# Performance work log

Hardware: AMD Instinct MI355X
Metric: run time of the kernel (lower is better)

## Reference

```python
import jax, jax.numpy as jnp
import numpy as np

N_NODES = 100_000
N_EDGES = 1_600_000
N_GRAPHS = 512
HID = 64
NUM_CLASSES = 100
VOCAB = 3100
ID_OFFSET = 1500
BN_EPS = 1e-5


def setup_inputs() -> dict:
    key = jax.random.key(0)
    ks = jax.random.split(key, 8)
    node_ids = jax.random.randint(ks[0], (N_NODES,), 0, 1600)
    edge_src = jax.random.randint(ks[1], (N_EDGES,), 0, N_NODES)
    edge_dst = jax.random.randint(ks[2], (N_EDGES,), 0, N_NODES)
    graph_ids = jnp.sort(jax.random.randint(ks[3], (N_NODES,), 0, N_GRAPHS))
    emb = jax.random.normal(ks[4], (VOCAB, HID), dtype=jnp.float32) * 0.02
    # 3 GIN layers x 3 MLP linear layers, all 64->64 since embedding_dim == hidden
    Ws = jax.random.normal(ks[5], (3, 3, HID, HID), dtype=jnp.float32) * 0.05
    bs = jnp.zeros((3, 3, HID), dtype=jnp.float32)
    bn_gamma = jnp.ones((3, HID), dtype=jnp.float32)
    bn_beta = jnp.zeros((3, HID), dtype=jnp.float32)
    eps = jnp.zeros((3,), dtype=jnp.float32)  # learn_eps=True, init 0
    W_out = jax.random.normal(ks[6], (3 * HID, NUM_CLASSES), dtype=jnp.float32) * 0.05
    b_out = jnp.zeros((NUM_CLASSES,), dtype=jnp.float32)
    return {"node_ids": node_ids, "edge_src": edge_src, "edge_dst": edge_dst,
            "graph_ids": graph_ids, "emb": emb, "Ws": Ws, "bs": bs,
            "bn_gamma": bn_gamma, "bn_beta": bn_beta, "eps": eps,
            "W_out": W_out, "b_out": b_out}


def reference(node_ids, edge_src, edge_dst, graph_ids, emb, Ws, bs,
              bn_gamma, bn_beta, eps, W_out, b_out):
    n = node_ids.shape[0]
    h = emb[node_ids + ID_OFFSET]  # [N, HID]
    pooled = []
    for l in range(3):  # GIN layers (fixed small count)
        # GINConv, sum aggregator: (1+eps)*h + sum over in-edges of h[src]
        agg = jax.ops.segment_sum(h[edge_src], edge_dst, num_segments=n)
        x = (1.0 + eps[l]) * h + agg
        for m in range(3):
            x = jax.nn.relu(x @ Ws[l, m] + bs[l, m])
        mean = x.mean(axis=0)
        var = x.var(axis=0)  # biased var, as torch BN uses for normalization
        x = (x - mean) * jax.lax.rsqrt(var + BN_EPS) * bn_gamma[l] + bn_beta[l]
        h = x
        # dgl.sum_nodes: per-graph segment sum
        pooled.append(jax.ops.segment_sum(h, graph_ids, num_segments=N_GRAPHS))
    graph_features = jnp.concatenate(pooled, axis=-1)  # [G, 3*HID]
    return graph_features @ W_out + b_out  # [G, NUM_CLASSES]
```

## Files before the change

### kernel.cpp

```cpp
#include <hip/hip_runtime.h>

#define N_NODES 100000
#define N_EDGES 1600000
#define N_GRAPHS 512
#define HID 64
#define NUM_CLASSES 100
#define ID_OFFSET 1500
#define BN_EPS 1e-5f
#define CAP 64
#define NBKT 256
#define BSHIFT 9
#define NUSED ((N_NODES + 511) >> 9)
#define BCAP 10240
#define CBLK 98
#define CHUNK 16384
#define WPBLK 5
#define EMBBLK ((N_NODES * 32 + 1023) / 1024)
#define DUMMY_ROW 100000

typedef __attribute__((ext_vector_type(8))) short short8;
typedef __attribute__((ext_vector_type(4))) float floatx4;

__device__ __forceinline__ float b2f(unsigned short u) {
    return __builtin_bit_cast(float, ((unsigned)u) << 16);
}
__device__ __forceinline__ unsigned short f2b(float f) {
    unsigned x = __builtin_bit_cast(unsigned, f);
    x += 0x7FFFu + ((x >> 16) & 1u);
    return (unsigned short)(x >> 16);
}

#define XSH(row, qq) ((((((row) >> 4) << 7) + ((qq) << 4) + (((row) & 15) ^ (qq))) * 8))


__global__ __launch_bounds__(1024) void prep_kernel(const int* __restrict__ src,
                                                    const int* __restrict__ dst,
                                                    int* __restrict__ cursor,
                                                    int* __restrict__ rec,
                                                    const float* __restrict__ Ws,
                                                    unsigned short* __restrict__ whi,
                                                    unsigned short* __restrict__ wlo,
                                                    const int* __restrict__ node_ids,
                                                    const int* __restrict__ gid,
                                                    const float* __restrict__ emb,
                                                    unsigned short* __restrict__ h,
                                                    unsigned short* __restrict__ xin,
                                                    int* __restrict__ gs,
                                                    int* __restrict__ ge) {
    __shared__ int hist[NBKT];
    __shared__ int base_s[NBKT];
    int t = threadIdx.x;
    int blk = blockIdx.x;

    if (blk < CBLK) {
        if (blk == 0 && t < 32) {
            ((unsigned*)(h + (size_t)DUMMY_ROW * 64))[t] = 0u;
            ((unsigned*)(xin + (size_t)DUMMY_ROW * 64))[t] = 0u;
        }
        if (t < NBKT) hist[t] = 0;
        __syncthreads();
        int cb = blk * CHUNK;
        int d_[16], s_[16];
#pragma unroll
        for (int k = 0; k < 16; ++k) {
            int i = cb + k * 1024 + t;
            d_[k] = (i < N_EDGES) ? dst[i] : -1;
            s_[k] = (i < N_EDGES) ? src[i] : 0;
            if (d_[k] >= 0) atomicAdd(&hist[((unsigned)d_[k] >> BSHIFT) & (NBKT - 1)], 1);
        }
        __syncthreads();
        if (t < NBKT) base_s[t] = (hist[t] > 0) ? atomicAdd(&cursor[t], hist[t]) : 0;
        __syncthreads();
        if (t < NBKT) hist[t] = 0;
        __syncthreads();
#pragma unroll
        for (int k = 0; k < 16; ++k) {
            if (d_[k] >= 0) {
                unsigned d = (unsigned)d_[k];
                int b = (d >> BSHIFT) & (NBKT - 1);
                int p = atomicAdd(&hist[b], 1);
                int g = base_s[b] + p;
                if ((unsigned)g < BCAP)
                    rec[b * BCAP + g] = ((int)(d & 511) << 17) | (s_[k] & 0x1FFFF);
            }
        }
    } else if (blk < CBLK + WPBLK) {
        int G = (blk - CBLK) * 1024 + t;
        if (G < 3 * 1536) {
            int l = G / 1536, Gp = G % 1536;
            int mm = Gp >> 9, rem = Gp & 511;
            int kq = rem >> 6, n = rem & 63;
            const float* Wp = Ws + l * 12288 + mm * 4096 + (kq * 8) * 64 + n;
            unsigned short uh[8], ul[8];
#pragma unroll
            for (int j = 0; j < 8; ++j) {
                float w = Wp[j * 64];
                unsigned short hi = f2b(w);
                uh[j] = hi;
                ul[j] = f2b(w - b2f(hi));
            }
            size_t off = (size_t)l * 12288 + (mm << 12) + XSH(n, kq);
            *(short8*)&whi[off] = *(short8*)uh;
            *(short8*)&wlo[off] = *(short8*)ul;
        }
    } else {
        int idx = (blk - CBLK - WPBLK) * 1024 + t;
        if (idx < N_NODES * 32) {
            int n = idx >> 5, cp = idx & 31;
            const float2 e = *(const float2*)(emb + (((size_t)(node_ids[n] + ID_OFFSET)) << 6) + cp * 2);
            unsigned v = (unsigned)f2b(e.x) | ((unsigned)f2b(e.y) << 16);
            ((unsigned*)h)[n * 32 + cp] = v;
            if (cp == 0) {
                int g = gid[n] & (N_GRAPHS - 1);
                if (n == 0 || (gid[n - 1] & (N_GRAPHS - 1)) != g) gs[g] = n;
                if (n == N_NODES - 1 || (gid[n + 1] & (N_GRAPHS - 1)) != g) ge[g] = n + 1;
            }
        }
    }
}


__global__ __launch_bounds__(1024) void fill_kernel(const int* __restrict__ rec,
                                                    const int* __restrict__ cursor,
                                                    int* __restrict__ cnt,
                                                    int* __restrict__ srcs) {
    __shared__ int lcnt[512];
    int t = threadIdx.x;
    int b = blockIdx.x;
    if (t < 512) lcnt[t] = 0;
    __syncthreads();
    int nb = cursor[b];
    if (nb < 0) nb = 0;
    if (nb > BCAP) nb = BCAP;
    const int* seg = rec + b * BCAP;
    for (int i = t; i < nb; i += 1024) {
        unsigned r = (unsigned)seg[i];
        int dl = (int)((r >> 17) & 511);
        int s = (int)(r & 0x1FFFF);
        int node = (b << BSHIFT) + dl;
        int p = atomicAdd(&lcnt[dl], 1);
        if (p < CAP && node < N_NODES) srcs[(node << 6) + p] = s;
    }
    __syncthreads();
    if (t < 512) {
        int node = (b << BSHIFT) + t;
        if (node < N_NODES) {
            int deg = lcnt[t];
            cnt[node] = deg;
            int degc = deg > CAP ? CAP : deg;
            int degp = (degc + 15) & ~15;
            if (degp < 32) degp = 32;
            for (int p = degc; p < degp; ++p) srcs[(node << 6) + p] = DUMMY_ROW;
        }
    }
}


__global__ __launch_bounds__(256, 4) void fused_kernel(const unsigned short* __restrict__ x,
                                                       unsigned short* __restrict__ xo,
                                                       const int* __restrict__ cnt,
                                                       const int* __restrict__ srcs,
                                                       const float* __restrict__ eps, int l,
                                                       float* __restrict__ stats,
                                                       const float* __restrict__ gamma,
                                                       const float* __restrict__ beta,
                                                       const unsigned short* __restrict__ whi,
                                                       const unsigned short* __restrict__ wlo,
                                                       const float* __restrict__ bs,
                                                       const int* __restrict__ graph_ids,
                                                       float* __restrict__ pooled, int last) {
    __shared__ __align__(16) unsigned short xs[64 * 64];
    __shared__ int garr[64];
    __shared__ float ssum[256], sqq[256];
    int t = threadIdx.x;
    int nodebase = blockIdx.x * 64;
    int lane = t & 63, w = t >> 6;
    int half = lane >> 5, cl = lane & 31;
    const unsigned* __restrict__ xu = (const unsigned*)x;

    if (lane < 16) {
        int n = nodebase + w * 16 + lane;
        garr[w * 16 + lane] = (n < N_NODES) ? (graph_ids[n] & (N_GRAPHS - 1)) : -1;
    }

    float scale = 1.0f + eps[l];
    float a0f = 1.0f, a1f = 1.0f, b0f = 0.0f, b1f = 0.0f;
    if (l > 0) {
        int lp = l - 1;
        float2 sm = *(const float2*)&stats[lp * 128 + 2 * cl];
        float2 sq = *(const float2*)&stats[lp * 128 + 64 + 2 * cl];
        float2 gm = *(const float2*)&gamma[lp * 64 + 2 * cl];
        float2 bt = *(const float2*)&beta[lp * 64 + 2 * cl];
        float mean0 = sm.x * (1.0f / N_NODES);
        float var0 = sq.x * (1.0f / N_NODES) - mean0 * mean0;
        float r0 = rsqrtf(var0 + BN_EPS);
        a0f = gm.x * r0;
        b0f = bt.x - mean0 * a0f;
        float mean1 = sm.y * (1.0f / N_NODES);
        float var1 = sq.y * (1.0f / N_NODES) - mean1 * mean1;
        float r1 = rsqrtf(var1 + BN_EPS);
        a1f = gm.y * r1;
        b1f = bt.y - mean1 * a1f;
    }

    int wb = __builtin_amdgcn_readfirstlane(nodebase + w * 16);

    for (int g4 = 0; g4 < 4; ++g4) {
        int nb = wb + g4 * 4;
        int deg[4], degp[4];
        const int* row[4];
#pragma unroll
        for (int n = 0; n < 4; ++n) {
            int d = (nb + n < N_NODES) ? cnt[nb + n] : 0;
            int dc = d < 0 ? 0 : (d > CAP ? CAP : d);
            deg[n] = dc;
            int dp = (dc + 15) & ~15;
            degp[n] = dp < 32 ? 32 : dp;
            row[n] = srcs + ((size_t)(nb + n) << 6);
        }
        int cmax = degp[0];
        cmax = degp[1] > cmax ? degp[1] : cmax;
        cmax = degp[2] > cmax ? degp[2] : cmax;
        cmax = degp[3] > cmax ? degp[3] : cmax;

        unsigned us[4];
#pragma unroll
        for (int n = 0; n < 4; ++n) us[n] = xu[(size_t)(nb + n) * 32 + cl];

        float A0[4] = {0.f, 0.f, 0.f, 0.f}, A1[4] = {0.f, 0.f, 0.f, 0.f};
        float B0[4] = {0.f, 0.f, 0.f, 0.f}, B1[4] = {0.f, 0.f, 0.f, 0.f};

        {
            unsigned uv[4][16];
#pragma unroll
            for (int n = 0; n < 4; ++n)
#pragma unroll
                for (int k = 0; k < 16; ++k) {
                    int ia = row[n][2 * k] & 0x1FFFF;
                    int ib = row[n][2 * k + 1] & 0x1FFFF;
                    int idx = half ? ib : ia;
                    uv[n][k] = xu[(size_t)idx * 32 + cl];
                }
#pragma unroll
            for (int n = 0; n < 4; ++n)
#pragma unroll
                for (int k = 0; k < 16; ++k) {
                    float lo = b2f((unsigned short)(uv[n][k] & 0xFFFF));
                    float hi = b2f((unsigned short)(uv[n][k] >> 16));
                    if (k & 1) { B0[n] += lo; B1[n] += hi; }
                    else       { A0[n] += lo; A1[n] += hi; }
                }
        }
        for (int c = 32; c < cmax; c += 16) {
            unsigned uc[4][8];
#pragma unroll
            for (int n = 0; n < 4; ++n)
                if (c < degp[n])
#pragma unroll
                    for (int k = 0; k < 8; ++k) {
                        int ia = row[n][c + 2 * k] & 0x1FFFF;
                        int ib = row[n][c + 2 * k + 1] & 0x1FFFF;
                        int idx = half ? ib : ia;
                        uc[n][k] = xu[(size_t)idx * 32 + cl];
                    }
#pragma unroll
            for (int n = 0; n < 4; ++n)
                if (c < degp[n])
#pragma unroll
                    for (int k = 0; k < 8; ++k) {
                        float lo = b2f((unsigned short)(uc[n][k] & 0xFFFF));
                        float hi = b2f((unsigned short)(uc[n][k] >> 16));
                        if (k & 1) { B0[n] += lo; B1[n] += hi; }
                        else       { A0[n] += lo; A1[n] += hi; }
                    }
        }

#pragma unroll
        for (int n = 0; n < 4; ++n) {
            float S0 = A0[n] + B0[n];
            float S1 = A1[n] + B1[n];
            S0 += __shfl_xor(S0, 32);
            S1 += __shfl_xor(S1, 32);
            if (half == 0) {
                float selflo = b2f((unsigned short)(us[n] & 0xFFFF));
                float selfhi = b2f((unsigned short)(us[n] >> 16));
                float db = scale + (float)deg[n];
                float v0 = fmaf(a0f, fmaf(scale, selflo, S0), db * b0f);
                float v1 = fmaf(a1f, fmaf(scale, selfhi, S1), db * b1f);
                int r = w * 16 + g4 * 4 + n;
                int col = 2 * cl;
                *(unsigned*)&xs[XSH(r, col >> 3) + (col & 7)] =
                    (unsigned)f2b(v0) | ((unsigned)f2b(v1) << 16);
            }
        }
    }

    int m = lane & 15, q = lane >> 4;
    const float* bb = bs + l * 3 * 64;
    const unsigned short* whil = whi + (size_t)l * 12288;
    const unsigned short* wlol = wlo + (size_t)l * 12288;
    for (int mm = 0; mm < 3; ++mm) {
        short8 bl[2][4];
#pragma unroll
        for (int kc = 0; kc < 2; ++kc)
#pragma unroll
            for (int tj = 0; tj < 4; ++tj)
                bl[kc][tj] = *(const short8*)&wlol[(mm << 12) + XSH(tj * 16 + m, kc * 4 + q)];
        short8 a[2];
#pragma unroll
        for (int kc = 0; kc < 2; ++kc)
            a[kc] = *(const short8*)&xs[XSH(w * 16 + m, kc * 4 + q)];

        floatx4 acc[4];
#pragma unroll
        for (int tj = 0; tj < 4; ++tj) {
            float bv = bb[mm * 64 + tj * 16 + m];
            acc[tj] = (floatx4){bv, bv, bv, bv};
        }
#pragma unroll
        for (int kc = 0; kc < 2; ++kc) {
            short8 bh[4];
#pragma unroll
            for (int tj = 0; tj < 4; ++tj)
                bh[tj] = *(const short8*)&whil[(mm << 12) + XSH(tj * 16 + m, kc * 4 + q)];
#pragma unroll
            for (int tj = 0; tj < 4; ++tj)
                acc[tj] = __builtin_amdgcn_mfma_f32_16x16x32_bf16(a[kc], bh[tj], acc[tj], 0, 0, 0);
        }
#pragma unroll
        for (int kc = 0; kc < 2; ++kc)
#pragma unroll
            for (int tj = 0; tj < 4; ++tj)
                acc[tj] = __builtin_amdgcn_mfma_f32_16x16x32_bf16(a[kc], bl[kc][tj], acc[tj], 0, 0, 0);
#pragma unroll
        for (int tj = 0; tj < 4; ++tj) {
            int col = tj * 16 + m;
#pragma unroll
            for (int r = 0; r < 4; ++r) {
                int row = w * 16 + q * 4 + r;
                float v = acc[tj][r];
                xs[XSH(row, col >> 3) + (col & 7)] = f2b(v > 0.f ? v : 0.f);
            }
        }
    }

    if (!last) {
        unsigned* xou = (unsigned*)xo;
#pragma unroll
        for (int it = 0; it < 8; ++it) {
            int row = w * 16 + (lane >> 5) + it * 2;
            int cp = lane & 31;
            int col = cp * 2;
            unsigned val = *(const unsigned*)&xs[XSH(row, col >> 3) + (col & 7)];
            int node = nodebase + row;
            if (node < N_NODES) xou[(size_t)node * 32 + cp] = val;
        }
    }
    {
        int c = lane;
        float s = 0.f, q2 = 0.f, acc2 = 0.f;
        int cur = -1;
        for (int k = 0; k < 16; ++k) {
            int row = w * 16 + k;
            int g = garr[row];
            if (g >= 0) {
                float v = b2f(xs[XSH(row, c >> 3) + (c & 7)]);
                s += v;
                q2 += v * v;
                if (g != cur) {
                    if (cur >= 0) atomicAdd(&pooled[cur * 192 + l * 64 + c], acc2);
                    acc2 = 0.f;
                    cur = g;
                }
                acc2 += v;
            }
        }
        if (cur >= 0) atomicAdd(&pooled[cur * 192 + l * 64 + c], acc2);
        ssum[t] = s;
        sqq[t] = q2;
    }
    __syncthreads();
    if (t < 64) {
        float S = ssum[t] + ssum[t + 64] + ssum[t + 128] + ssum[t + 192];
        float Q = sqq[t] + sqq[t + 64] + sqq[t + 128] + sqq[t + 192];
        atomicAdd(&stats[l * 128 + t], S);
        atomicAdd(&stats[l * 128 + 64 + t], Q);
    }
}


__global__ __launch_bounds__(256) void out_kernel(const float* __restrict__ pooled,
                                                  const float* __restrict__ stats,
                                                  const float* __restrict__ gamma,
                                                  const float* __restrict__ beta,
                                                  const int* __restrict__ gs,
                                                  const int* __restrict__ ge,
                                                  const float* __restrict__ Wo,
                                                  const float* __restrict__ bo,
                                                  float* __restrict__ out) {
    __shared__ float sab[384];
    int t = threadIdx.x;
    if (t < 192) {
        int l2 = t / 64, c = t & 63;
        float mean = stats[l2 * 128 + c] * (1.0f / N_NODES);
        float var = stats[l2 * 128 + 64 + c] * (1.0f / N_NODES) - mean * mean;
        float rstd = rsqrtf(var + BN_EPS);
        float a = gamma[l2 * 64 + c] * rstd;
        sab[l2 * 128 + c] = a;
        sab[l2 * 128 + 64 + c] = beta[l2 * 64 + c] - mean * a;
    }
    __syncthreads();
    int idx = blockIdx.x * blockDim.x + t;
    if (idx < N_GRAPHS * NUM_CLASSES) {
        int g = idx / NUM_CLASSES, k = idx % NUM_CLASSES;
        float cg = (float)(ge[g] - gs[g]);
        float acc = bo[k];
        for (int l2 = 0; l2 < 3; ++l2)
            for (int c = 0; c < 64; ++c) {
                float gf = fmaf(sab[l2 * 128 + c], pooled[g * 192 + l2 * 64 + c],
                                sab[l2 * 128 + 64 + c] * cg);
                acc = fmaf(gf, Wo[(l2 * 64 + c) * NUM_CLASSES + k], acc);
            }
        out[idx] = acc;
    }
}

extern "C" void kernel_launch(void* const* d_in, const int* in_sizes, int n_in,
                              void* d_out, int out_size, void* d_ws, size_t ws_size,
                              hipStream_t stream) {
    const int*   node_ids  = (const int*)d_in[0];
    const int*   edge_src  = (const int*)d_in[1];
    const int*   edge_dst  = (const int*)d_in[2];
    const int*   graph_ids = (const int*)d_in[3];
    const float* emb       = (const float*)d_in[4];
    const float* Ws        = (const float*)d_in[5];
    const float* bs        = (const float*)d_in[6];
    const float* gamma     = (const float*)d_in[7];
    const float* beta      = (const float*)d_in[8];
    const float* eps       = (const float*)d_in[9];
    const float* W_out     = (const float*)d_in[10];
    const float* b_out     = (const float*)d_in[11];
    float* out = (float*)d_out;

    unsigned short* h    = (unsigned short*)d_ws;
    unsigned short* xin  = h + 6400000 + 8192;
    unsigned short* whi  = xin + 6400000 + 8192;
    unsigned short* wlo  = whi + 36864;
    int*   srcs   = (int*)(wlo + 36864);
    int*   rec    = srcs + 6400000;
    float* pooled = (float*)(rec + NUSED * BCAP);
    float* stats  = pooled + 98304;
    int*   cnt    = (int*)(stats + 384);
    int*   gs     = cnt + 100000;
    int*   ge     = gs + 512;
    int*   cursor = ge + 512;

    hipMemsetAsync(pooled, 0,
                   (size_t)(98304 + 384 + 100000 + 512 + 512 + 256) * 4, stream);

    prep_kernel<<<CBLK + WPBLK + EMBBLK, 1024, 0, stream>>>(
        edge_src, edge_dst, cursor, rec, Ws, whi, wlo,
        node_ids, graph_ids, emb, h, xin, gs, ge);
    fill_kernel<<<NUSED, 1024, 0, stream>>>(rec, cursor, cnt, srcs);

    const int FUSE_BLK = (N_NODES + 63) / 64;
    for (int l = 0; l < 3; ++l) {
        const unsigned short* X = (l % 2 == 0) ? h : xin;
        unsigned short* A = (l % 2 == 0) ? xin : h;
        fused_kernel<<<FUSE_BLK, 256, 0, stream>>>(
            X, A, cnt, srcs, eps, l, stats, gamma, beta,
            whi, wlo, bs, graph_ids, pooled, l == 2);
    }

    out_kernel<<<(N_GRAPHS * NUM_CLASSES + 255) / 256, 256, 0, stream>>>(
        pooled, stats, gamma, beta, gs, ge, W_out, b_out, out);
}
```

Measured before the change: 349.4 us.

## Shrink fused GIN blocks to 16 nodes and replicate BN stat accumulators

Each fused block now handles 16 nodes instead of 64, so there are four times as many blocks, more parallelism and a smaller LDS footprint. The MLP is restructured so all four waves compute column tiles of a single 16-row tile, with double-buffered LDS and barriers between stages, and only one wave writes each result. BatchNorm sum and sum-of-squares atomics are spread over 16 replicated accumulators to reduce contention, and readers sum the replicas. The cost is redundant MFMA work across waves, extra __syncthreads, and four times as many stat atomics and prologue loads.

```diff
diff --git a/kernel.cpp b/kernel.cpp
--- a/kernel.cpp
+++ b/kernel.cpp
@@ -17,6 +17,8 @@
 #define WPBLK 5
 #define EMBBLK ((N_NODES * 32 + 1023) / 1024)
 #define DUMMY_ROW 100000
+#define SREP 16
+#define SSTRIDE 384
 
 typedef __attribute__((ext_vector_type(8))) short short8;
 typedef __attribute__((ext_vector_type(4))) float floatx4;
@@ -169,49 +171,52 @@
                                                        const float* __restrict__ bs,
                                                        const int* __restrict__ graph_ids,
                                                        float* __restrict__ pooled, int last) {
-    __shared__ __align__(16) unsigned short xs[64 * 64];
-    __shared__ int garr[64];
+    __shared__ __align__(16) unsigned short xs[2 * 16 * 64];
+    __shared__ int garr[16];
     __shared__ float ssum[256], sqq[256];
     int t = threadIdx.x;
-    int nodebase = blockIdx.x * 64;
+    int nodebase = blockIdx.x * 16;
     int lane = t & 63, w = t >> 6;
     int half = lane >> 5, cl = lane & 31;
     const unsigned* __restrict__ xu = (const unsigned*)x;
 
-    if (lane < 16) {
-        int n = nodebase + w * 16 + lane;
-        garr[w * 16 + lane] = (n < N_NODES) ? (graph_ids[n] & (N_GRAPHS - 1)) : -1;
-    }
+    if (t < 16) garr[t] = graph_ids[nodebase + t] & (N_GRAPHS - 1);
 
     float scale = 1.0f + eps[l];
     float a0f = 1.0f, a1f = 1.0f, b0f = 0.0f, b1f = 0.0f;
     if (l > 0) {
         int lp = l - 1;
-        float2 sm = *(const float2*)&stats[lp * 128 + 2 * cl];
-        float2 sq = *(const float2*)&stats[lp * 128 + 64 + 2 * cl];
+        float sm0 = 0.f, sm1 = 0.f, sq0 = 0.f, sq1 = 0.f;
+#pragma unroll
+        for (int rp = 0; rp < SREP; ++rp) {
+            const float* sp = stats + rp * SSTRIDE + lp * 128;
+            float2 a_ = *(const float2*)&sp[2 * cl];
+            float2 b_ = *(const float2*)&sp[64 + 2 * cl];
+            sm0 += a_.x; sm1 += a_.y;
+            sq0 += b_.x; sq1 += b_.y;
+        }
         float2 gm = *(const float2*)&gamma[lp * 64 + 2 * cl];
         float2 bt = *(const float2*)&beta[lp * 64 + 2 * cl];
-        float mean0 = sm.x * (1.0f / N_NODES);
-        float var0 = sq.x * (1.0f / N_NODES) - mean0 * mean0;
+        float mean0 = sm0 * (1.0f / N_NODES);
+        float var0 = sq0 * (1.0f / N_NODES) - mean0 * mean0;
         float r0 = rsqrtf(var0 + BN_EPS);
         a0f = gm.x * r0;
         b0f = bt.x - mean0 * a0f;
-        float mean1 = sm.y * (1.0f / N_NODES);
-        float var1 = sq.y * (1.0f / N_NODES) - mean1 * mean1;
+        float mean1 = sm1 * (1.0f / N_NODES);
+        float var1 = sq1 * (1.0f / N_NODES) - mean1 * mean1;
         float r1 = rsqrtf(var1 + BN_EPS);
         a1f = gm.y * r1;
         b1f = bt.y - mean1 * a1f;
     }
 
-    int wb = __builtin_amdgcn_readfirstlane(nodebase + w * 16);
-
-    for (int g4 = 0; g4 < 4; ++g4) {
-        int nb = wb + g4 * 4;
+    int nb = __builtin_amdgcn_readfirstlane(nodebase + w * 4);
+
+    {
         int deg[4], degp[4];
         const int* row[4];
 #pragma unroll
         for (int n = 0; n < 4; ++n) {
-            int d = (nb + n < N_NODES) ? cnt[nb + n] : 0;
+            int d = cnt[nb + n];
             int dc = d < 0 ? 0 : (d > CAP ? CAP : d);
             deg[n] = dc;
             int dp = (dc + 15) & ~15;
@@ -287,19 +292,22 @@
                 float db = scale + (float)deg[n];
                 float v0 = fmaf(a0f, fmaf(scale, selflo, S0), db * b0f);
                 float v1 = fmaf(a1f, fmaf(scale, selfhi, S1), db * b1f);
-                int r = w * 16 + g4 * 4 + n;
+                int r = w * 4 + n;
                 int col = 2 * cl;
                 *(unsigned*)&xs[XSH(r, col >> 3) + (col & 7)] =
                     (unsigned)f2b(v0) | ((unsigned)f2b(v1) << 16);
             }
         }
     }
+    __syncthreads();
 
     int m = lane & 15, q = lane >> 4;
     const float* bb = bs + l * 3 * 64;
     const unsigned short* whil = whi + (size_t)l * 12288;
     const unsigned short* wlol = wlo + (size_t)l * 12288;
     for (int mm = 0; mm < 3; ++mm) {
+        unsigned short* xr = xs + (mm & 1) * 1024;
+        unsigned short* xw = xs + ((mm & 1) ^ 1) * 1024;
         short8 bl[2][4];
 #pragma unroll
         for (int kc = 0; kc < 2; ++kc)
@@ -309,7 +317,7 @@
         short8 a[2];
 #pragma unroll
         for (int kc = 0; kc < 2; ++kc)
-            a[kc] = *(const short8*)&xs[XSH(w * 16 + m, kc * 4 + q)];
+            a[kc] = *(const short8*)&xr[XSH(m, kc * 4 + q)];
 
         floatx4 acc[4];
 #pragma unroll
@@ -335,45 +343,48 @@
 #pragma unroll
         for (int tj = 0; tj < 4; ++tj) {
             int col = tj * 16 + m;
-#pragma unroll
-            for (int r = 0; r < 4; ++r) {
-                int row = w * 16 + q * 4 + r;
-                float v = acc[tj][r];
-                xs[XSH(row, col >> 3) + (col & 7)] = f2b(v > 0.f ? v : 0.f);
-            }
-        }
-    }
+            if (q == w) {
+#pragma unroll
+                for (int r = 0; r < 4; ++r) {
+                    int row = q * 4 + r;
+                    float v = acc[tj][r];
+                    xw[XSH(row, col >> 3) + (col & 7)] = f2b(v > 0.f ? v : 0.f);
+                }
+            }
+        }
+        __syncthreads();
+    }
+
+    unsigned short* xf = xs + 1024;
 
     if (!last) {
         unsigned* xou = (unsigned*)xo;
 #pragma unroll
-        for (int it = 0; it < 8; ++it) {
-            int row = w * 16 + (lane >> 5) + it * 2;
+        for (int it = 0; it < 2; ++it) {
+            int row = w * 4 + (lane >> 5) + it * 2;
             int cp = lane & 31;
             int col = cp * 2;
-            unsigned val = *(const unsigned*)&xs[XSH(row, col >> 3) + (col & 7)];
-            int node = nodebase + row;
-            if (node < N_NODES) xou[(size_t)node * 32 + cp] = val;
+            unsigned val = *(const unsigned*)&xf[XSH(row, col >> 3) + (col & 7)];
+            xou[(size_t)(nodebase + row) * 32 + cp] = val;
         }
     }
     {
         int c = lane;
         float s = 0.f, q2 = 0.f, acc2 = 0.f;
         int cur = -1;
-        for (int k = 0; k < 16; ++k) {
-            int row = w * 16 + k;
+#pragma unroll
+        for (int k = 0; k < 4; ++k) {
+            int row = w * 4 + k;
             int g = garr[row];
-            if (g >= 0) {
-                float v = b2f(xs[XSH(row, c >> 3) + (c & 7)]);
-                s += v;
-                q2 += v * v;
-                if (g != cur) {
-                    if (cur >= 0) atomicAdd(&pooled[cur * 192 + l * 64 + c], acc2);
-                    acc2 = 0.f;
-                    cur = g;
-                }
-                acc2 += v;
-            }
+            float v = b2f(xf[XSH(row, c >> 3) + (c & 7)]);
+            s += v;
+            q2 += v * v;
+            if (g != cur) {
+                if (cur >= 0) atomicAdd(&pooled[cur * 192 + l * 64 + c], acc2);
+                acc2 = 0.f;
+                cur = g;
+            }
+            acc2 += v;
         }
         if (cur >= 0) atomicAdd(&pooled[cur * 192 + l * 64 + c], acc2);
         ssum[t] = s;
@@ -383,8 +394,9 @@
     if (t < 64) {
         float S = ssum[t] + ssum[t + 64] + ssum[t + 128] + ssum[t + 192];
         float Q = sqq[t] + sqq[t + 64] + sqq[t + 128] + sqq[t + 192];
-        atomicAdd(&stats[l * 128 + t], S);
-        atomicAdd(&stats[l * 128 + 64 + t], Q);
+        float* sp = stats + (blockIdx.x & (SREP - 1)) * SSTRIDE + l * 128;
+        atomicAdd(&sp[t], S);
+        atomicAdd(&sp[64 + t], Q);
     }
 }
 
@@ -402,8 +414,14 @@
     int t = threadIdx.x;
     if (t < 192) {
         int l2 = t / 64, c = t & 63;
-        float mean = stats[l2 * 128 + c] * (1.0f / N_NODES);
-        float var = stats[l2 * 128 + 64 + c] * (1.0f / N_NODES) - mean * mean;
+        float S = 0.f, Q = 0.f;
+#pragma unroll
+        for (int rp = 0; rp < SREP; ++rp) {
+            S += stats[rp * SSTRIDE + l2 * 128 + c];
+            Q += stats[rp * SSTRIDE + l2 * 128 + 64 + c];
+        }
+        float mean = S * (1.0f / N_NODES);
+        float var = Q * (1.0f / N_NODES) - mean * mean;
         float rstd = rsqrtf(var + BN_EPS);
         float a = gamma[l2 * 64 + c] * rstd;
         sab[l2 * 128 + c] = a;
@@ -450,20 +468,20 @@
     int*   rec    = srcs + 6400000;
     float* pooled = (float*)(rec + NUSED * BCAP);
     float* stats  = pooled + 98304;
-    int*   cnt    = (int*)(stats + 384);
+    int*   cnt    = (int*)(stats + SREP * SSTRIDE);
     int*   gs     = cnt + 100000;
     int*   ge     = gs + 512;
     int*   cursor = ge + 512;
 
     hipMemsetAsync(pooled, 0,
-                   (size_t)(98304 + 384 + 100000 + 512 + 512 + 256) * 4, stream);
+                   (size_t)(98304 + SREP * SSTRIDE + 100000 + 512 + 512 + 256) * 4, stream);
 
     prep_kernel<<<CBLK + WPBLK + EMBBLK, 1024, 0, stream>>>(
         edge_src, edge_dst, cursor, rec, Ws, whi, wlo,
         node_ids, graph_ids, emb, h, xin, gs, ge);
     fill_kernel<<<NUSED, 1024, 0, stream>>>(rec, cursor, cnt, srcs);
 
-    const int FUSE_BLK = (N_NODES + 63) / 64;
+    const int FUSE_BLK = N_NODES / 16;
     for (int l = 0; l < 3; ++l) {
         const unsigned short* X = (l % 2 == 0) ? h : xin;
         unsigned short* A = (l % 2 == 0) ? xin : h;
```

Result: slower. 393.5 us (+12.6%).
